# Kernel tuning notes

Hardware: AMD Instinct MI355X
Metric: run time of the kernel (lower is better)

The kernel has to match this reference:

```python
import jax, jax.numpy as jnp
import numpy as np


def relu_bt(x):
    # -threshold(-leaky_relu(x), -t, -t) == min(leaky_relu(x), t), t = ||x||_inf (detached)
    t = jax.lax.stop_gradient(jnp.max(jnp.abs(x)))
    return jnp.minimum(jax.nn.leaky_relu(x, negative_slope=0.01), t)


def setup_inputs() -> dict:
    key = jax.random.key(0)
    k1, k2, k3, k4 = jax.random.split(key, 4)
    N, E, F_in, F_out = 100000, 1600000, 128, 64
    x = jax.random.normal(k1, (N, F_in), dtype=jnp.float32)
    edge_index = jax.random.randint(k2, (2, E), 0, N, dtype=jnp.int64)
    # xavier_normal with gain=1.414
    W = jax.random.normal(k3, (F_in, F_out), dtype=jnp.float32) * (1.414 * np.sqrt(2.0 / (F_in + F_out)))
    a = jax.random.normal(k4, (1, 4 * F_out), dtype=jnp.float32) * (1.414 * np.sqrt(2.0 / (1 + 4 * F_out)))
    return {"x": x, "edge_index": edge_index, "W": W, "a": a}


def reference(x, edge_index, W, a):
    N = x.shape[0]
    F_out = W.shape[1]
    h = x @ W  # [N, F_out]
    src = edge_index[0]
    dst = edge_index[1]
    hs = h[src]  # [E, F_out]
    hd = h[dst]  # [E, F_out]
    agg = relu_bt(hs + hd)
    diff = relu_bt(hs - hd)
    # a @ cat([hs, hd, agg, diff], dim=1).T == sum of four per-edge dot products
    a0, a1, a2, a3 = jnp.split(a.reshape(4 * F_out), 4)
    score = hs @ a0 + hd @ a1 + agg @ a2 + diff @ a3  # [E]
    edge_e = jnp.exp(-relu_bt(score))  # [E]
    # spmm(A, ones): rowsum over outgoing edges (grouped by src)
    e_rowsum = jax.ops.segment_sum(edge_e, src, num_segments=N)  # [N]
    # spmm(A, h): weighted aggregation of neighbor (dst) features into src rows
    h_prime = jax.ops.segment_sum(edge_e[:, None] * hd, src, num_segments=N)  # [N, F_out]
    return h_prime / (e_rowsum[:, None] + 1e-16)
```

## Files before the change

kernel.cpp:

```cpp
#include <hip/hip_runtime.h>
#include <hip/hip_fp16.h>

#define F_IN 128
#define F_OUT 64
#define BIN_TILE 2048
#define BSHIFT 5
#define BNODES 32
#define BCAP 1024u

#define LK_A 0.505f
#define LK_B 0.495f

__device__ __forceinline__ float leaky(float v) {
    return fmaf(LK_B, fabsf(v), LK_A * v);
}

template <int CTRL>
__device__ __forceinline__ float dppadd(float v) {
    return v + __builtin_bit_cast(float,
        __builtin_amdgcn_update_dpp(0, __builtin_bit_cast(int, v), CTRL, 0xf, 0xf, true));
}

__device__ __forceinline__ float sum8(float v) {
    v = dppadd<0xB1>(v);
    v = dppadd<0x4E>(v);
    v = dppadd<0x141>(v);
    return v;
}

__device__ __forceinline__ float xslot_sum2(float v) {
    v = dppadd<0x128>(v);
    v += __shfl_xor(v, 16);
    return v;
}

__device__ __forceinline__ float wave_sum(float v) {
    v += __builtin_bit_cast(float, __builtin_amdgcn_update_dpp(0, __builtin_bit_cast(int, v), 0x111, 0xf, 0xf, true));
    v += __builtin_bit_cast(float, __builtin_amdgcn_update_dpp(0, __builtin_bit_cast(int, v), 0x112, 0xf, 0xf, true));
    v += __builtin_bit_cast(float, __builtin_amdgcn_update_dpp(0, __builtin_bit_cast(int, v), 0x114, 0xf, 0xe, true));
    v += __builtin_bit_cast(float, __builtin_amdgcn_update_dpp(0, __builtin_bit_cast(int, v), 0x118, 0xf, 0xc, true));
    v += __builtin_bit_cast(float, __builtin_amdgcn_update_dpp(0, __builtin_bit_cast(int, v), 0x142, 0xa, 0xf, true));
    v += __builtin_bit_cast(float, __builtin_amdgcn_update_dpp(0, __builtin_bit_cast(int, v), 0x143, 0xc, 0xf, true));
    return __builtin_bit_cast(float, __builtin_amdgcn_readlane(__builtin_bit_cast(int, v), 63));
}

__device__ __forceinline__ void cvt8(const uint4 u, float* g) {
    float2 f;
    f = __half22float2(__builtin_bit_cast(__half2, u.x)); g[0] = f.x; g[1] = f.y;
    f = __half22float2(__builtin_bit_cast(__half2, u.y)); g[2] = f.x; g[3] = f.y;
    f = __half22float2(__builtin_bit_cast(__half2, u.z)); g[4] = f.x; g[5] = f.y;
    f = __half22float2(__builtin_bit_cast(__half2, u.w)); g[6] = f.x; g[7] = f.y;
}

__device__ __forceinline__ float4 cvt4h(const uint2 u) {
    const float2 f0 = __half22float2(__builtin_bit_cast(__half2, u.x));
    const float2 f1 = __half22float2(__builtin_bit_cast(__half2, u.y));
    return make_float4(f0.x, f0.y, f1.x, f1.y);
}

__global__ __launch_bounds__(256) void gemm_binA(const float* __restrict__ x,
                                                 const float* __restrict__ W,
                                                 float* __restrict__ h32,
                                                 uint2* __restrict__ h16,
                                                 const int* __restrict__ ei,
                                                 unsigned* __restrict__ gcur,
                                                 unsigned* __restrict__ binned,
                                                 int N, int E, int NB, int ngemm,
                                                 unsigned cap, int mode) {
    __shared__ unsigned smem_u[4096];

    if ((int)blockIdx.x < ngemm) {
        __half2* wl = (__half2*)smem_u;
        for (int i = threadIdx.x; i < F_IN * F_OUT / 2; i += 256) {
            const float2 f = ((const float2*)W)[i];
            wl[i] = __floats2half2_rn(f.x, f.y);
        }
        __syncthreads();

        const int cg = threadIdx.x & 15;
        const int rs = threadIdx.x >> 4;
        const int row0 = blockIdx.x * 128 + rs * 8;

        int r[8];
#pragma unroll
        for (int i = 0; i < 8; ++i) { const int rr = row0 + i; r[i] = rr < N ? rr : N - 1; }

        float4 acc[8];
#pragma unroll
        for (int i = 0; i < 8; ++i) acc[i] = make_float4(0.f, 0.f, 0.f, 0.f);

        float4 xc[8];
#pragma unroll
        for (int i = 0; i < 8; ++i) xc[i] = *(const float4*)(x + (size_t)r[i] * F_IN);

        const char* wbase = (const char*)smem_u;
        for (int k4 = 0; k4 < 32; ++k4) {
            float4 xn[8];
            if (k4 < 31) {
#pragma unroll
                for (int i = 0; i < 8; ++i)
                    xn[i] = *(const float4*)(x + (size_t)r[i] * F_IN + (k4 + 1) * 4);
            }
            float4 wv[4];
#pragma unroll
            for (int kk = 0; kk < 4; ++kk) {
                const uint2 u = *(const uint2*)(wbase + ((k4 * 4 + kk) * 64 + cg * 4) * 2);
                wv[kk] = cvt4h(u);
            }

#pragma unroll
            for (int i = 0; i < 8; ++i) {
                acc[i].x = fmaf(xc[i].x, wv[0].x, acc[i].x);
                acc[i].y = fmaf(xc[i].x, wv[0].y, acc[i].y);
                acc[i].z = fmaf(xc[i].x, wv[0].z, acc[i].z);
                acc[i].w = fmaf(xc[i].x, wv[0].w, acc[i].w);
                acc[i].x = fmaf(xc[i].y, wv[1].x, acc[i].x);
                acc[i].y = fmaf(xc[i].y, wv[1].y, acc[i].y);
                acc[i].z = fmaf(xc[i].y, wv[1].z, acc[i].z);
                acc[i].w = fmaf(xc[i].y, wv[1].w, acc[i].w);
                acc[i].x = fmaf(xc[i].z, wv[2].x, acc[i].x);
                acc[i].y = fmaf(xc[i].z, wv[2].y, acc[i].y);
                acc[i].z = fmaf(xc[i].z, wv[2].z, acc[i].z);
                acc[i].w = fmaf(xc[i].z, wv[2].w, acc[i].w);
                acc[i].x = fmaf(xc[i].w, wv[3].x, acc[i].x);
                acc[i].y = fmaf(xc[i].w, wv[3].y, acc[i].y);
                acc[i].z = fmaf(xc[i].w, wv[3].z, acc[i].z);
                acc[i].w = fmaf(xc[i].w, wv[3].w, acc[i].w);
            }
            if (k4 < 31) {
#pragma unroll
                for (int i = 0; i < 8; ++i) xc[i] = xn[i];
            }
        }

#pragma unroll
        for (int i = 0; i < 8; ++i) {
            const int rr = row0 + i;
            if (rr < N) {
                if (mode & 2) *(float4*)(h32 + (size_t)rr * F_OUT + cg * 4) = acc[i];
                if (mode & 1) {
                    uint2 u;
                    u.x = __builtin_bit_cast(unsigned, __floats2half2_rn(acc[i].x, acc[i].y));
                    u.y = __builtin_bit_cast(unsigned, __floats2half2_rn(acc[i].z, acc[i].w));
                    h16[(size_t)rr * 16 + cg] = u;
                }
            }
        }
    } else {
        unsigned* lcnt = smem_u;
        const int t = threadIdx.x;
        for (int i = t; i < NB; i += 256) lcnt[i] = 0;
        __syncthreads();
        const int base = ((int)blockIdx.x - ngemm) * BIN_TILE;
        unsigned pk[8], bk[8], rk[8];
#pragma unroll
        for (int i = 0; i < 8; ++i) {
            const int e = base + i * 256 + t;
            if (e < E) {
                const unsigned s = (unsigned)ei[e];
                const unsigned d = (unsigned)ei[E + e];
                bk[i] = s >> BSHIFT;
                pk[i] = ((s & (BNODES - 1u)) << 17) | d;
                rk[i] = atomicAdd(&lcnt[bk[i]], 1u);
            }
        }
        __syncthreads();
        for (int i = t; i < NB; i += 256) {
            const unsigned c = lcnt[i];
            lcnt[i] = c ? atomicAdd(&gcur[i], c) : 0u;
        }
        __syncthreads();
#pragma unroll
        for (int i = 0; i < 8; ++i) {
            const int e = base + i * 256 + t;
            if (e < E) {
                const unsigned po = lcnt[bk[i]] + rk[i];
                if (po < cap) binned[(size_t)bk[i] * cap + po] = pk[i];
            }
        }
    }
}

__global__ __launch_bounds__(256) void bucket_node(const unsigned* __restrict__ binned,
                                                   const unsigned* __restrict__ gcur,
                                                   const uint2* __restrict__ h16v,
                                                   const float* __restrict__ a,
                                                   float* __restrict__ out,
                                                   int N, unsigned cap) {
    __shared__ unsigned stg[BCAP];
    __shared__ uint4    hsl[BNODES * 8];
    __shared__ unsigned ndeg[BNODES];
    __shared__ unsigned nbase[BNODES];
    __shared__ unsigned ncur[BNODES];

    const int b = blockIdx.x;
    const int t = threadIdx.x;
    const int node0 = b << BSHIFT;
    const size_t src0 = (size_t)b * cap;
    unsigned sz = gcur[b]; if (sz > cap) sz = cap;

    if (t < BNODES) ndeg[t] = 0;
    {
        const uint4* hsrc = (const uint4*)h16v;
        const int limit = N * 8;
        const int gi = node0 * 8 + t;
        hsl[t] = (gi < limit) ? hsrc[gi] : make_uint4(0u, 0u, 0u, 0u);
    }
    __syncthreads();

    for (unsigned i = t; i < sz; i += 256)
        atomicAdd(&ndeg[binned[src0 + i] >> 17], 1u);
    __syncthreads();

    if (t < BNODES) {
        const unsigned d = ndeg[t];
        unsigned sc = d;
#pragma unroll
        for (int st = 1; st < BNODES; st <<= 1) {
            const unsigned o = __shfl_up(sc, st, 64);
            if (t >= st) sc += o;
        }
        nbase[t] = sc - d;
        ncur[t]  = sc - d;
    }
    __syncthreads();

    for (unsigned i = t; i < sz; i += 256) {
        const unsigned p = binned[src0 + i];
        const unsigned pos = atomicAdd(&ncur[p >> 17], 1u);
        stg[pos] = p & 0x1FFFFu;
    }
    __syncthreads();

    const int lane  = t & 63;
    const int half  = lane >> 5;
    const int slot4 = (lane >> 3) & 3;
    const int q     = lane & 7;
    const int slot8 = (t >> 6) * 2 + half;
    const char* h16 = (const char*)h16v;

    float b1[8], a2b[8], a3b[8], a0m[8];
#pragma unroll
    for (int f = 0; f < 8; ++f) {
        const float A0 = a[q * 8 + f];
        const float A1 = a[64 + q * 8 + f];
        const float A2 = a[128 + q * 8 + f];
        const float A3 = a[192 + q * 8 + f];
        b1[f]  = fmaf(LK_A, A2 - A3, A1);
        a2b[f] = LK_B * A2;
        a3b[f] = LK_B * A3;
        a0m[f] = fmaf(LK_A, A2 + A3, A0);
    }

#pragma unroll 1
    for (int nn = 0; nn < BNODES / 8; ++nn) {
        const int nloc = slot8 * (BNODES / 8) + nn;
        const int node = node0 + nloc;
        const int beg = (int)nbase[nloc];
        const int len = (int)ndeg[nloc];

        float hs[8]; cvt8(hsl[nloc * 8 + q], hs);
        float csp = 0.f;
#pragma unroll
        for (int f = 0; f < 8; ++f) csp = fmaf(hs[f], a0m[f], csp);
        const float cs = sum8(csp);

        float acc[8];
#pragma unroll
        for (int f = 0; f < 8; ++f) acc[f] = 0.f;
        float rsum = 0.f;

        const int lm1 = (len > 0) ? len - 1 : 0;
        int dA = 0;
        if (len > 0) { int e0 = slot4; if (e0 > lm1) e0 = lm1; dA = (int)stg[beg + e0]; }
        uint4 uA = *(const uint4*)(h16 + ((size_t)dA << 7) + q * 16);
        int dB = dA;
        if (len > 4) { int e1 = 4 + slot4; if (e1 > lm1) e1 = lm1; dB = (int)stg[beg + e1]; }
        uint4 uB = *(const uint4*)(h16 + ((size_t)dB << 7) + q * 16);
        int dC = dB;
        if (len > 8) { int e2 = 8 + slot4; if (e2 > lm1) e2 = lm1; dC = (int)stg[beg + e2]; }

        for (int cb = 0; cb < len; cb += 4) {
            uint4 uC = uB;
            int dD = dC;
            if (cb + 8 < len)
                uC = *(const uint4*)(h16 + ((size_t)dC << 7) + q * 16);
            if (cb + 12 < len) { int e3 = cb + 12 + slot4; if (e3 > lm1) e3 = lm1; dD = (int)stg[beg + e3]; }

            float g[8];
            cvt8(uA, g);
            float p0 = 0.f, p1 = 0.f;
#pragma unroll
            for (int f = 0; f < 8; f += 2) {
                const float sa0 = hs[f] + g[f],         sb0 = hs[f] - g[f];
                const float sa1 = hs[f + 1] + g[f + 1], sb1 = hs[f + 1] - g[f + 1];
                p0 = fmaf(g[f],     b1[f],     p0);
                p1 = fmaf(g[f + 1], b1[f + 1], p1);
                p0 = fmaf(fabsf(sa0), a2b[f],     p0);
                p1 = fmaf(fabsf(sa1), a2b[f + 1], p1);
                p0 = fmaf(fabsf(sb0), a3b[f],     p0);
                p1 = fmaf(fabsf(sb1), a3b[f + 1], p1);
            }
            const float R = sum8(p0 + p1);

            float e = __expf(-leaky(cs + R));
            e = (cb + slot4 < len) ? e : 0.f;
#pragma unroll
            for (int f = 0; f < 8; ++f) acc[f] = fmaf(e, g[f], acc[f]);
            rsum += e;

            uA = uB; uB = uC; dC = dD;
        }

#pragma unroll
        for (int f = 0; f < 8; ++f) acc[f] = xslot_sum2(acc[f]);
        rsum = xslot_sum2(rsum);

        if (slot4 == 0 && node < N) {
            const float inv = 1.f / (rsum + 1e-16f);
            float4 o0, o1;
            o0.x = acc[0] * inv; o0.y = acc[1] * inv; o0.z = acc[2] * inv; o0.w = acc[3] * inv;
            o1.x = acc[4] * inv; o1.y = acc[5] * inv; o1.z = acc[6] * inv; o1.w = acc[7] * inv;
            float* orow = out + (size_t)node * F_OUT + q * 8;
            *(float4*)orow = o0;
            *(float4*)(orow + 4) = o1;
        }
    }
}

__global__ __launch_bounds__(256) void hist_kernel(const int* __restrict__ ei,
                                                   unsigned* __restrict__ cnt, int E) {
    const int e = blockIdx.x * 256 + threadIdx.x;
    if (e < E) atomicAdd(&cnt[ei[e]], 1u);
}

__global__ __launch_bounds__(256) void scan1(const unsigned* __restrict__ cnt,
                                             unsigned* __restrict__ bsum, int n) {
    __shared__ unsigned lds[256];
    const int t = threadIdx.x;
    const int base = blockIdx.x * 2048 + t * 8;
    unsigned s = 0;
#pragma unroll
    for (int i = 0; i < 8; ++i) { const int idx = base + i; if (idx < n) s += cnt[idx]; }
    lds[t] = s; __syncthreads();
    for (int st = 128; st > 0; st >>= 1) {
        if (t < st) lds[t] += lds[t + st];
        __syncthreads();
    }
    if (t == 0) bsum[blockIdx.x] = lds[0];
}

__global__ __launch_bounds__(128) void scan2(unsigned* __restrict__ bsum,
                                             unsigned* __restrict__ off, int nb, int n) {
    __shared__ unsigned lds[128];
    const int t = threadIdx.x;
    if (t < nb) lds[t] = bsum[t];
    __syncthreads();
    if (t == 0) {
        unsigned run = 0;
        for (int i = 0; i < nb; ++i) { const unsigned v = lds[i]; lds[i] = run; run += v; }
        off[n] = run;
    }
    __syncthreads();
    if (t < nb) bsum[t] = lds[t];
}

__global__ __launch_bounds__(256) void scan3(const unsigned* __restrict__ cnt,
                                             const unsigned* __restrict__ bsum,
                                             unsigned* __restrict__ off,
                                             unsigned* __restrict__ cursor, int n) {
    __shared__ unsigned lds[256];
    const int t = threadIdx.x;
    const int base = blockIdx.x * 2048 + t * 8;
    unsigned v[8]; unsigned s = 0;
#pragma unroll
    for (int i = 0; i < 8; ++i) { const int idx = base + i; v[i] = (idx < n) ? cnt[idx] : 0u; s += v[i]; }
    lds[t] = s; __syncthreads();
    for (int st = 1; st < 256; st <<= 1) {
        const unsigned add = (t >= st) ? lds[t - st] : 0u;
        __syncthreads();
        lds[t] += add;
        __syncthreads();
    }
    unsigned excl = (t > 0 ? lds[t - 1] : 0u) + bsum[blockIdx.x];
#pragma unroll
    for (int i = 0; i < 8; ++i) {
        const int idx = base + i;
        if (idx < n) { off[idx] = excl; cursor[idx] = excl; excl += v[i]; }
    }
}

__global__ __launch_bounds__(256) void scatter_kernel(const int* __restrict__ ei,
                                                      unsigned* __restrict__ cursor,
                                                      int* __restrict__ sdst, int E) {
    const int e = blockIdx.x * 256 + threadIdx.x;
    if (e >= E) return;
    const int s = ei[e];
    const int d = ei[E + e];
    const unsigned pos = atomicAdd(&cursor[s], 1u);
    sdst[pos] = d;
}

__global__ __launch_bounds__(256) void node_kernel(const unsigned* __restrict__ off,
                                                   const unsigned* __restrict__ deg,
                                                   const int* __restrict__ sdst,
                                                   const uint2* __restrict__ h16v,
                                                   const float* __restrict__ a,
                                                   float* __restrict__ out, int N) {
    const int lane  = threadIdx.x & 63;
    const int half  = lane >> 5;
    const int slot4 = (lane >> 3) & 3;
    const int q     = lane & 7;
    const char* h16 = (const char*)h16v;

    float b1[8], a2b[8], a3b[8], a0m[8];
#pragma unroll
    for (int f = 0; f < 8; ++f) {
        const float A0 = a[q * 8 + f];
        const float A1 = a[64 + q * 8 + f];
        const float A2 = a[128 + q * 8 + f];
        const float A3 = a[192 + q * 8 + f];
        b1[f]  = fmaf(LK_A, A2 - A3, A1);
        a2b[f] = LK_B * A2;
        a3b[f] = LK_B * A3;
        a0m[f] = fmaf(LK_A, A2 + A3, A0);
    }

    const int wid = (int)((blockIdx.x * 256u + threadIdx.x) >> 6);
    const int nw  = (int)((gridDim.x * 256u) >> 6);

    for (int pr = wid; pr * 2 < N; pr += nw) {
        const int node = pr * 2 + half;
        const int nc = (node < N) ? node : N - 1;
        const unsigned beg = off[nc];
        const int len = (node < N) ? (int)deg[nc] : 0;

        float hs[8];
        cvt8(*(const uint4*)(h16 + ((size_t)nc << 7) + q * 16), hs);
        float csp = 0.f;
#pragma unroll
        for (int f = 0; f < 8; ++f) csp = fmaf(hs[f], a0m[f], csp);
        const float cs = sum8(csp);

        const int lenO = __shfl_xor(len, 32);
        const int ml = (len > lenO) ? len : lenO;

        float acc[8];
#pragma unroll
        for (int f = 0; f < 8; ++f) acc[f] = 0.f;
        float rsum = 0.f;

        const int lm1 = (len > 0) ? len - 1 : 0;
        int dA = 0;
        if (len > 0) { int e0 = slot4; if (e0 > lm1) e0 = lm1; dA = sdst[beg + e0]; }
        uint4 uA = *(const uint4*)(h16 + ((size_t)dA << 7) + q * 16);
        int dB = dA;
        if (len > 4) { int e1 = 4 + slot4; if (e1 > lm1) e1 = lm1; dB = sdst[beg + e1]; }
        uint4 uB = *(const uint4*)(h16 + ((size_t)dB << 7) + q * 16);
        int dC = dB;
        if (len > 8) { int e2 = 8 + slot4; if (e2 > lm1) e2 = lm1; dC = sdst[beg + e2]; }

        for (int cb = 0; cb < ml; cb += 4) {
            uint4 uC = uB;
            int dD = dC;
            if (cb + 8 < len)
                uC = *(const uint4*)(h16 + ((size_t)dC << 7) + q * 16);
            if (cb + 12 < len) { int e3 = cb + 12 + slot4; if (e3 > lm1) e3 = lm1; dD = sdst[beg + e3]; }

            float g[8];
            cvt8(uA, g);
            float p0 = 0.f, p1 = 0.f;
#pragma unroll
            for (int f = 0; f < 8; f += 2) {
                const float sa0 = hs[f] + g[f],         sb0 = hs[f] - g[f];
                const float sa1 = hs[f + 1] + g[f + 1], sb1 = hs[f + 1] - g[f + 1];
                p0 = fmaf(g[f],     b1[f],     p0);
                p1 = fmaf(g[f + 1], b1[f + 1], p1);
                p0 = fmaf(fabsf(sa0), a2b[f],     p0);
                p1 = fmaf(fabsf(sa1), a2b[f + 1], p1);
                p0 = fmaf(fabsf(sb0), a3b[f],     p0);
                p1 = fmaf(fabsf(sb1), a3b[f + 1], p1);
            }
            const float R = sum8(p0 + p1);
            float e = __expf(-leaky(cs + R));
            e = (cb + slot4 < len) ? e : 0.f;
#pragma unroll
            for (int f = 0; f < 8; ++f) acc[f] = fmaf(e, g[f], acc[f]);
            rsum += e;
            uA = uB; uB = uC; dC = dD;
        }

#pragma unroll
        for (int f = 0; f < 8; ++f) acc[f] = xslot_sum2(acc[f]);
        rsum = xslot_sum2(rsum);

        if (slot4 == 0 && node < N) {
            const float inv = 1.f / (rsum + 1e-16f);
            float4 o0, o1;
            o0.x = acc[0] * inv; o0.y = acc[1] * inv; o0.z = acc[2] * inv; o0.w = acc[3] * inv;
            o1.x = acc[4] * inv; o1.y = acc[5] * inv; o1.z = acc[6] * inv; o1.w = acc[7] * inv;
            float* orow = out + (size_t)node * F_OUT + q * 8;
            *(float4*)orow = o0;
            *(float4*)(orow + 4) = o1;
        }
    }
}

__device__ __forceinline__ float edge_part(float hs, float hd, float a1, float a2, float a3) {
    float p = hd * a1;
    p = fmaf(leaky(hs + hd), a2, p);
    p = fmaf(leaky(hs - hd), a3, p);
    return p;
}

__global__ __launch_bounds__(256) void edge_kernel(const int* __restrict__ ei,
                                                   const float* __restrict__ h,
                                                   const float* __restrict__ a,
                                                   float* __restrict__ hprime,
                                                   float* __restrict__ rowsum,
                                                   int E) {
    const int lane = threadIdx.x & 63;
    const int wave = (int)((blockIdx.x * blockDim.x + threadIdx.x) >> 6);
    const int nwaves = (int)((gridDim.x * blockDim.x) >> 6);
    const float a0 = a[lane], a1 = a[64 + lane], a2 = a[128 + lane], a3 = a[192 + lane];
    for (int e = wave; e < E; e += nwaves) {
        const int s = ei[e];
        const int d = ei[E + e];
        const float hs = h[(size_t)s * F_OUT + lane];
        const float hd = h[(size_t)d * F_OUT + lane];
        const float part = wave_sum(hs * a0 + edge_part(hs, hd, a1, a2, a3));
        const float ee = __expf(-leaky(part));
        atomicAdd(&hprime[(size_t)s * F_OUT + lane], ee * hd);
        if (lane == 0) atomicAdd(&rowsum[s], ee);
    }
}

__global__ __launch_bounds__(256) void finalize(float* __restrict__ out,
                                                const float* __restrict__ rowsum,
                                                int total) {
    const int i = blockIdx.x * blockDim.x + threadIdx.x;
    if (i < total) out[i] = out[i] / (rowsum[i >> 6] + 1e-16f);
}

static inline size_t align_up(size_t v, size_t a) { return (v + a - 1) & ~(a - 1); }

extern "C" void kernel_launch(void* const* d_in, const int* in_sizes, int n_in,
                              void* d_out, int out_size, void* d_ws, size_t ws_size,
                              hipStream_t stream) {
    const float* x  = (const float*)d_in[0];
    const int*   ei = (const int*)d_in[1];
    const float* W  = (const float*)d_in[2];
    const float* a  = (const float*)d_in[3];

    const int N = in_sizes[0] / F_IN;
    const int E = in_sizes[1] / 2;
    float* out = (float*)d_out;

    const int NB = (N + BNODES - 1) >> BSHIFT;
    const int ngemm = (N + 127) / 128;
    const int nbt = (E + BIN_TILE - 1) / BIN_TILE;
    const unsigned meanFill = (NB > 0) ? (unsigned)(E / NB) : 0u;

    char* ws = (char*)d_ws;
    const size_t szh16  = align_up((size_t)N * F_OUT * 2, 256);
    const size_t szoff  = align_up(((size_t)N + 1) * 4, 256);
    const size_t szedge = align_up((size_t)E * 4 + 64, 256);
    const size_t szbin  = align_up((size_t)NB * BCAP * 4 + 64, 256);

    const size_t binned_b = szh16;
    const size_t gcurA_b  = binned_b + szbin;
    const size_t needA    = gcurA_b + align_up((size_t)NB * 4, 256);
    const size_t offB_b   = szh16;
    const size_t degB_b   = offB_b + szoff;
    const size_t sdstB_b  = degB_b + szoff;
    const size_t cursor_b = sdstB_b + szedge;
    const size_t bsum_b   = cursor_b + align_up((size_t)N * 4, 256);
    const size_t needB    = bsum_b + 4096;

    uint2* h16 = (uint2*)ws;

    if (ws_size >= needA && N <= (1 << 17) && NB <= 4096 && meanFill <= (BCAP * 3u) / 4u) {
        unsigned* binned = (unsigned*)(ws + binned_b);
        unsigned* gcur   = (unsigned*)(ws + gcurA_b);

        hipMemsetAsync(gcur, 0, (size_t)NB * 4, stream);
        gemm_binA<<<ngemm + nbt, 256, 0, stream>>>(x, W, nullptr, h16, ei, gcur, binned,
                                                   N, E, NB, ngemm, BCAP, 1);
        bucket_node<<<NB, 256, 0, stream>>>(binned, gcur, h16, a, out, N, BCAP);
    } else if (ws_size >= needB && N <= (1 << 17)) {
        unsigned* off    = (unsigned*)(ws + offB_b);
        unsigned* deg    = (unsigned*)(ws + degB_b);
        int*      sdst   = (int*)(ws + sdstB_b);
        unsigned* cursor = (unsigned*)(ws + cursor_b);
        unsigned* bsum   = (unsigned*)(ws + bsum_b);
        const int nb2 = (N + 2047) / 2048;

        hipMemsetAsync(deg, 0, (size_t)N * 4, stream);
        gemm_binA<<<ngemm, 256, 0, stream>>>(x, W, nullptr, h16, ei, nullptr, nullptr,
                                             N, E, NB, ngemm, BCAP, 1);
        hist_kernel<<<(E + 255) / 256, 256, 0, stream>>>(ei, deg, E);
        scan1<<<nb2, 256, 0, stream>>>(deg, bsum, N);
        scan2<<<1, 128, 0, stream>>>(bsum, off, nb2, N);
        scan3<<<nb2, 256, 0, stream>>>(deg, bsum, off, cursor, N);
        scatter_kernel<<<(E + 255) / 256, 256, 0, stream>>>(ei, cursor, sdst, E);
        node_kernel<<<2048, 256, 0, stream>>>(off, deg, sdst, h16, a, out, N);
    } else {
        float* h32    = (float*)ws;
        float* rowsum = (float*)(ws + align_up((size_t)N * F_OUT * 4, 256));
        hipMemsetAsync(d_out, 0, (size_t)N * F_OUT * sizeof(float), stream);
        hipMemsetAsync(rowsum, 0, (size_t)N * sizeof(float), stream);
        gemm_binA<<<ngemm, 256, 0, stream>>>(x, W, h32, nullptr, ei, nullptr, nullptr,
                                             N, E, NB, ngemm, BCAP, 2);
        edge_kernel<<<2048, 256, 0, stream>>>(ei, h32, a, out, rowsum, E);
        finalize<<<((size_t)N * F_OUT + 255) / 256, 256, 0, stream>>>(out, rowsum, N * F_OUT);
    }
}
```

Baseline: 135.2 us.

## Keep W in fp32 LDS for GEMM and double bucket_node threads to 512

Measured after the change: 136.5 us. No clear change (+1.0%).

```diff
diff --git a/kernel.cpp b/kernel.cpp
--- a/kernel.cpp
+++ b/kernel.cpp
@@ -50,12 +50,6 @@
     f = __half22float2(__builtin_bit_cast(__half2, u.y)); g[2] = f.x; g[3] = f.y;
     f = __half22float2(__builtin_bit_cast(__half2, u.z)); g[4] = f.x; g[5] = f.y;
     f = __half22float2(__builtin_bit_cast(__half2, u.w)); g[6] = f.x; g[7] = f.y;
-}
-
-__device__ __forceinline__ float4 cvt4h(const uint2 u) {
-    const float2 f0 = __half22float2(__builtin_bit_cast(__half2, u.x));
-    const float2 f1 = __half22float2(__builtin_bit_cast(__half2, u.y));
-    return make_float4(f0.x, f0.y, f1.x, f1.y);
 }
 
 __global__ __launch_bounds__(256) void gemm_binA(const float* __restrict__ x,
@@ -67,13 +61,14 @@
                                                  unsigned* __restrict__ binned,
                                                  int N, int E, int NB, int ngemm,
                                                  unsigned cap, int mode) {
-    __shared__ unsigned smem_u[4096];
+    __shared__ unsigned smem_u[8192];
 
     if ((int)blockIdx.x < ngemm) {
-        __half2* wl = (__half2*)smem_u;
-        for (int i = threadIdx.x; i < F_IN * F_OUT / 2; i += 256) {
-            const float2 f = ((const float2*)W)[i];
-            wl[i] = __floats2half2_rn(f.x, f.y);
+        float (*w_lds)[F_OUT] = (float (*)[F_OUT])smem_u;
+        {
+            const float4* Wv = (const float4*)W;
+            float4* wl = (float4*)w_lds;
+            for (int i = threadIdx.x; i < F_IN * F_OUT / 4; i += 256) wl[i] = Wv[i];
         }
         __syncthreads();
 
@@ -93,7 +88,6 @@
 #pragma unroll
         for (int i = 0; i < 8; ++i) xc[i] = *(const float4*)(x + (size_t)r[i] * F_IN);
 
-        const char* wbase = (const char*)smem_u;
         for (int k4 = 0; k4 < 32; ++k4) {
             float4 xn[8];
             if (k4 < 31) {
@@ -103,10 +97,8 @@
             }
             float4 wv[4];
 #pragma unroll
-            for (int kk = 0; kk < 4; ++kk) {
-                const uint2 u = *(const uint2*)(wbase + ((k4 * 4 + kk) * 64 + cg * 4) * 2);
-                wv[kk] = cvt4h(u);
-            }
+            for (int kk = 0; kk < 4; ++kk)
+                wv[kk] = *(const float4*)&w_lds[k4 * 4 + kk][cg * 4];
 
 #pragma unroll
             for (int i = 0; i < 8; ++i) {
@@ -147,7 +139,8 @@
             }
         }
     } else {
-        unsigned* lcnt = smem_u;
+        unsigned* lcnt  = smem_u;
+        unsigned* lbase = smem_u + NB;
         const int t = threadIdx.x;
         for (int i = t; i < NB; i += 256) lcnt[i] = 0;
         __syncthreads();
@@ -167,21 +160,21 @@
         __syncthreads();
         for (int i = t; i < NB; i += 256) {
             const unsigned c = lcnt[i];
-            lcnt[i] = c ? atomicAdd(&gcur[i], c) : 0u;
+            lbase[i] = c ? atomicAdd(&gcur[i], c) : 0u;
         }
         __syncthreads();
 #pragma unroll
         for (int i = 0; i < 8; ++i) {
             const int e = base + i * 256 + t;
             if (e < E) {
-                const unsigned po = lcnt[bk[i]] + rk[i];
+                const unsigned po = lbase[bk[i]] + rk[i];
                 if (po < cap) binned[(size_t)bk[i] * cap + po] = pk[i];
             }
         }
     }
 }
 
-__global__ __launch_bounds__(256) void bucket_node(const unsigned* __restrict__ binned,
+__global__ __launch_bounds__(512) void bucket_node(const unsigned* __restrict__ binned,
                                                    const unsigned* __restrict__ gcur,
                                                    const uint2* __restrict__ h16v,
                                                    const float* __restrict__ a,
@@ -200,7 +193,7 @@
     unsigned sz = gcur[b]; if (sz > cap) sz = cap;
 
     if (t < BNODES) ndeg[t] = 0;
-    {
+    if (t < BNODES * 8) {
         const uint4* hsrc = (const uint4*)h16v;
         const int limit = N * 8;
         const int gi = node0 * 8 + t;
@@ -208,7 +201,7 @@
     }
     __syncthreads();
 
-    for (unsigned i = t; i < sz; i += 256)
+    for (unsigned i = t; i < sz; i += 512)
         atomicAdd(&ndeg[binned[src0 + i] >> 17], 1u);
     __syncthreads();
 
@@ -225,7 +218,7 @@
     }
     __syncthreads();
 
-    for (unsigned i = t; i < sz; i += 256) {
+    for (unsigned i = t; i < sz; i += 512) {
         const unsigned p = binned[src0 + i];
         const unsigned pos = atomicAdd(&ncur[p >> 17], 1u);
         stg[pos] = p & 0x1FFFFu;
@@ -236,7 +229,7 @@
     const int half  = lane >> 5;
     const int slot4 = (lane >> 3) & 3;
     const int q     = lane & 7;
-    const int slot8 = (t >> 6) * 2 + half;
+    const int proc  = (t >> 6) * 2 + half;
     const char* h16 = (const char*)h16v;
 
     float b1[8], a2b[8], a3b[8], a0m[8];
@@ -253,8 +246,8 @@
     }
 
 #pragma unroll 1
-    for (int nn = 0; nn < BNODES / 8; ++nn) {
-        const int nloc = slot8 * (BNODES / 8) + nn;
+    for (int nn = 0; nn < BNODES / 16; ++nn) {
+        const int nloc = proc * (BNODES / 16) + nn;
         const int node = node0 + nloc;
         const int beg = (int)nbase[nloc];
         const int len = (int)ndeg[nloc];
@@ -586,7 +579,7 @@
         hipMemsetAsync(gcur, 0, (size_t)NB * 4, stream);
         gemm_binA<<<ngemm + nbt, 256, 0, stream>>>(x, W, nullptr, h16, ei, gcur, binned,
                                                    N, E, NB, ngemm, BCAP, 1);
-        bucket_node<<<NB, 256, 0, stream>>>(binned, gcur, h16, a, out, N, BCAP);
+        bucket_node<<<NB, 512, 0, stream>>>(binned, gcur, h16, a, out, N, BCAP);
     } else if (ws_size >= needB && N <= (1 << 17)) {
         unsigned* off    = (unsigned*)(ws + offB_b);
         unsigned* deg    = (unsigned*)(ws + degB_b);
```
